# Optimization experiments

Measured on AMD Instinct MI355X. Metric: run time of the kernel, lower is better.

Reference implementation:

```python
import jax, jax.numpy as jnp
import numpy as np

EPS = 1e-7
MAX_TAN_NORM = 10.0  # safe_expmap0 clamp


def logmap0(x):
    # x: [..., D] Lorentz point, x[..., 0] = time component (>= 1)
    x0 = x[..., :1]
    xs = x[..., 1:]
    d = jnp.arccosh(jnp.clip(x0, 1.0 + EPS, None))          # geodesic distance to origin
    ns = jnp.clip(jnp.linalg.norm(xs, axis=-1, keepdims=True), EPS, None)
    return jnp.concatenate([jnp.zeros_like(x0), d * xs / ns], axis=-1)


def safe_expmap0(u):
    # u: tangent at origin; time component is projected out (proju at origin)
    us = u[..., 1:]
    n = jnp.clip(jnp.linalg.norm(us, axis=-1, keepdims=True), EPS, None)
    nc = jnp.minimum(n, MAX_TAN_NORM)                        # clamp norm for stability
    usc = us * (nc / n)
    return jnp.concatenate([jnp.cosh(nc), jnp.sinh(nc) * usc / nc], axis=-1)


def projx(x):
    # re-project onto the hyperboloid: x0 = sqrt(1 + ||xs||^2)
    xs = x[..., 1:]
    x0 = jnp.sqrt(1.0 + jnp.sum(xs * xs, axis=-1, keepdims=True))
    return jnp.concatenate([x0, xs], axis=-1)


def lorentz_linear(x_hyp, W, b):
    t = logmap0(x_hyp)
    y = t @ W.T + b
    return projx(safe_expmap0(y))


def setup_inputs() -> dict:
    key = jax.random.key(0)
    ks = jax.random.split(key, 8)
    N, D_IN, D_HID, D_OUT = 8192, 1024, 4096, 1024
    s = 0.02
    x_sp = jax.random.normal(ks[0], (N, D_IN), dtype=jnp.float32)
    x_hyp = projx(x_sp)  # valid Lorentz point (time comp overwritten)
    W1 = jax.random.normal(ks[1], (D_HID, D_IN), dtype=jnp.float32) * s
    b1 = jnp.zeros((D_HID,), dtype=jnp.float32)
    W2 = jax.random.normal(ks[2], (D_HID, D_HID), dtype=jnp.float32) * s
    b2 = jnp.zeros((D_HID,), dtype=jnp.float32)
    W3 = jax.random.normal(ks[3], (D_OUT, D_HID), dtype=jnp.float32) * s
    b3 = jnp.zeros((D_OUT,), dtype=jnp.float32)
    return {"x_hyp": x_hyp, "W1": W1, "b1": b1, "W2": W2, "b2": b2, "W3": W3, "b3": b3}


def reference(x_hyp, W1, b1, W2, b2, W3, b3):
    # layers[:-1] with inter-layer logmap0 -> (dropout=identity in eval) -> expmap0 -> projx
    h = lorentz_linear(x_hyp, W1, b1)
    h = projx(safe_expmap0(logmap0(h)))
    h = lorentz_linear(h, W2, b2)
    h = projx(safe_expmap0(logmap0(h)))
    return lorentz_linear(h, W3, b3)
```

## Files before the change

### kernel.cpp

```cpp
#include <hip/hip_runtime.h>
#include <stdint.h>

#define EPSF 1e-7f
#define MAXTAN 10.0f

typedef __bf16 bf16x8 __attribute__((ext_vector_type(8)));
typedef float floatx4 __attribute__((ext_vector_type(4)));
typedef __attribute__((address_space(3))) void lds_void_t;
typedef __attribute__((address_space(1))) void gbl_void_t;

__device__ __forceinline__ unsigned short f2bf(float x) {
  union { float f; uint32_t u; } v; v.f = x;
  uint32_t u = v.u;
  u += 0x7fffu + ((u >> 16) & 1u);
  return (unsigned short)(u >> 16);
}
__device__ __forceinline__ float bf2f(unsigned short h) {
  union { uint32_t u; float f; } v; v.u = ((uint32_t)h) << 16;
  return v.f;
}

__global__ void k_sniff(const unsigned short* __restrict__ x, int* __restrict__ mode) {
  if (threadIdx.x == 0 && blockIdx.x == 0) {
    int sane = 0;
    for (int i = 0; i < 128; ++i) {
      unsigned short h = x[i];
      int e = (h >> 7) & 0xFF;
      if ((h & 0x7FFF) == 0 || (e >= 96 && e <= 140)) ++sane;
    }
    *mode = (sane >= 120) ? 1 : 0;
  }
}

__global__ void k_zero(float* __restrict__ p, int n) {
  int i = blockIdx.x * 256 + threadIdx.x;
  if (i < n) p[i] = 0.f;
}

__global__ void k_cvtw(const void* __restrict__ in, unsigned short* __restrict__ out,
                       const int* __restrict__ mode, int n8) {
  int i = blockIdx.x * 256 + threadIdx.x;
  if (i >= n8) return;
  if (*mode) {
    ((uint4*)out)[i] = ((const uint4*)in)[i];
  } else {
    float4 a = ((const float4*)in)[2 * i];
    float4 b = ((const float4*)in)[2 * i + 1];
    ushort4 oa, ob;
    oa.x = f2bf(a.x); oa.y = f2bf(a.y); oa.z = f2bf(a.z); oa.w = f2bf(a.w);
    ob.x = f2bf(b.x); ob.y = f2bf(b.y); ob.z = f2bf(b.z); ob.w = f2bf(b.w);
    ((ushort4*)out)[2 * i] = oa;
    ((ushort4*)out)[2 * i + 1] = ob;
  }
}

__global__ void k_col0(const unsigned short* __restrict__ W, int K,
                       float* __restrict__ out, int n) {
  int i = blockIdx.x * 256 + threadIdx.x;
  if (i < n) out[i] = bf2f(W[(size_t)i * K]);
}

__global__ void k_logmap0(const void* __restrict__ xv, unsigned short* __restrict__ t,
                          const int* __restrict__ mode) {
  const int row = blockIdx.x;
  const int tid = threadIdx.x;
  float4 v; float x0;
  if (*mode) {
    const unsigned short* xr = (const unsigned short*)xv + (size_t)row * 1024;
    ushort4 u = ((const ushort4*)xr)[tid];
    v.x = bf2f(u.x); v.y = bf2f(u.y); v.z = bf2f(u.z); v.w = bf2f(u.w);
    x0 = bf2f(xr[0]);
  } else {
    const float* xr = (const float*)xv + (size_t)row * 1024;
    v = ((const float4*)xr)[tid];
    x0 = xr[0];
  }
  float s = v.x * v.x + v.y * v.y + v.z * v.z + v.w * v.w;
  if (tid == 0) s -= v.x * v.x;
  for (int off = 32; off; off >>= 1) s += __shfl_down(s, off, 64);
  __shared__ float red[4];
  if ((tid & 63) == 0) red[tid >> 6] = s;
  __syncthreads();
  s = red[0] + red[1] + red[2] + red[3];
  float ns = fmaxf(sqrtf(s), EPSF);
  float d = acoshf(fmaxf(x0, 1.0f + EPSF));
  float sc = d / ns;
  ushort4 o;
  o.x = f2bf(v.x * sc); o.y = f2bf(v.y * sc);
  o.z = f2bf(v.z * sc); o.w = f2bf(v.w * sc);
  if (tid == 0) o.x = 0;
  ((ushort4*)(t + (size_t)row * 1024))[tid] = o;
}

__global__ void k_sc(const float* __restrict__ ss, const unsigned short* __restrict__ y,
                     int stride, float* __restrict__ sc, float* __restrict__ c0f, int nrows) {
  int i = blockIdx.x * 256 + threadIdx.x;
  if (i >= nrows) return;
  float n = fmaxf(sqrtf(fmaxf(ss[i], 0.f)), EPSF);
  sc[i] = fminf(n, MAXTAN) / n;
  c0f[i] = bf2f(y[(size_t)i * stride]);
}

__global__ void k_final(const unsigned short* __restrict__ y, const float* __restrict__ ss,
                        void* __restrict__ outv, const int* __restrict__ mode) {
  const int row = blockIdx.x;
  const int tid = threadIdx.x;
  float n = fmaxf(sqrtf(fmaxf(ss[row], 0.f)), EPSF);
  float nc = fminf(n, MAXTAN);
  float a = sinhf(nc) / n;
  ushort4 u = ((const ushort4*)(y + (size_t)row * 1024))[tid];
  float4 o;
  o.x = bf2f(u.x) * a; o.y = bf2f(u.y) * a;
  o.z = bf2f(u.z) * a; o.w = bf2f(u.w) * a;
  if (tid == 0) o.x = coshf(nc);
  if (*mode) {
    ushort4 o16;
    o16.x = f2bf(o.x); o16.y = f2bf(o.y); o16.z = f2bf(o.z); o16.w = f2bf(o.w);
    ((ushort4*)outv)[(size_t)row * 256 + tid] = o16;
  } else {
    ((float4*)outv)[(size_t)row * 256 + tid] = o;
  }
}

template<int N, int K, bool CORR>
__global__ __launch_bounds__(256) void k_gemm_bt(
    const unsigned short* __restrict__ A,
    const unsigned short* __restrict__ B,
    const float* __restrict__ bias,
    const float* __restrict__ sc,
    const float* __restrict__ c0f,
    const float* __restrict__ wc0,
    unsigned short* __restrict__ Cb,
    float* __restrict__ ss)
{
  __shared__ __align__(16) unsigned short As[128 * 64];
  __shared__ __align__(16) unsigned short Bs[128 * 64];

  const int tid  = threadIdx.x;
  const int wave = tid >> 6;
  const int lane = tid & 63;
  const int quad = lane >> 4;
  const int m16  = lane & 15;

  const int bm = blockIdx.y * 128;
  const int bn = blockIdx.x * 128;

  const int srow = lane >> 3;
  const int gcol = (((lane & 7) ^ srow) << 3);

  const int wm = (wave >> 1) << 6;
  const int wn = (wave & 1) << 6;

  floatx4 acc[4][4];
#pragma unroll
  for (int i = 0; i < 4; ++i)
#pragma unroll
    for (int j = 0; j < 4; ++j)
#pragma unroll
      for (int r = 0; r < 4; ++r) acc[i][j][r] = 0.0f;

  for (int k0 = 0; k0 < K; k0 += 64) {
#pragma unroll
    for (int i = 0; i < 4; ++i) {
      const int rbase = wave * 32 + i * 8;
      const unsigned short* ga = A + (size_t)(bm + rbase + srow) * K + k0 + gcol;
      const unsigned short* gb = B + (size_t)(bn + rbase + srow) * K + k0 + gcol;
      __builtin_amdgcn_global_load_lds((gbl_void_t*)(void*)ga,
                                       (lds_void_t*)(As + rbase * 64), 16, 0, 0);
      __builtin_amdgcn_global_load_lds((gbl_void_t*)(void*)gb,
                                       (lds_void_t*)(Bs + rbase * 64), 16, 0, 0);
    }
    __syncthreads();

#pragma unroll
    for (int j = 0; j < 2; ++j) {
      bf16x8 af[4], bfg[4];
#pragma unroll
      for (int t = 0; t < 4; ++t) {
        const int gsw = (((j * 4 + quad) ^ (m16 & 7)) << 3);
        af[t]  = *(const bf16x8*)(As + (wm + t * 16 + m16) * 64 + gsw);
        bfg[t] = *(const bf16x8*)(Bs + (wn + t * 16 + m16) * 64 + gsw);
      }
#pragma unroll
      for (int mt = 0; mt < 4; ++mt)
#pragma unroll
        for (int nt = 0; nt < 4; ++nt)
          acc[mt][nt] = __builtin_amdgcn_mfma_f32_16x16x32_bf16(af[mt], bfg[nt], acc[mt][nt], 0, 0, 0);
    }
    __syncthreads();
  }

#pragma unroll
  for (int mt = 0; mt < 4; ++mt) {
#pragma unroll
    for (int r = 0; r < 4; ++r) {
      const int gm = bm + wm + mt * 16 + quad * 4 + r;
      float scv = 1.f, c0v = 0.f;
      if (CORR) { scv = sc[gm]; c0v = c0f[gm]; }
      float sq = 0.f;
#pragma unroll
      for (int nt = 0; nt < 4; ++nt) {
        const int gn = bn + wn + nt * 16 + m16;
        float v = acc[mt][nt][r];
        if (CORR) v = scv * (v - c0v * wc0[gn]);
        v += bias[gn];
        Cb[(size_t)gm * N + gn] = f2bf(v);
        sq += (gn == 0) ? 0.f : v * v;
      }
      sq += __shfl_xor(sq, 1, 64);
      sq += __shfl_xor(sq, 2, 64);
      sq += __shfl_xor(sq, 4, 64);
      sq += __shfl_xor(sq, 8, 64);
      if (m16 == 0) atomicAdd(&ss[gm], sq);
    }
  }
}

extern "C" void kernel_launch(void* const* d_in, const int* in_sizes, int n_in,
                              void* d_out, int out_size, void* d_ws, size_t ws_size,
                              hipStream_t stream) {
  const void* x  = d_in[0];
  const void* W1 = d_in[1];
  const float* b1 = (const float*)d_in[2];
  const void* W2 = d_in[3];
  const float* b2 = (const float*)d_in[4];
  const void* W3 = d_in[5];
  const float* b3 = (const float*)d_in[6];

  const int NR = 8192, DIN = 1024, DH = 4096, DOUT = 1024;

  char* ws = (char*)d_ws;
  size_t off = 0;
  int* mode = (int*)(ws + off);               off += 256;
  unsigned short* W1b = (unsigned short*)(ws + off); off += (size_t)DH * DIN * 2;
  unsigned short* W2b = (unsigned short*)(ws + off); off += (size_t)DH * DH * 2;
  unsigned short* W3b = (unsigned short*)(ws + off); off += (size_t)DOUT * DH * 2;
  unsigned short* t1  = (unsigned short*)(ws + off); off += (size_t)NR * DIN * 2;
  unsigned short* y1  = (unsigned short*)(ws + off); off += (size_t)NR * DH * 2;
  unsigned short* y2  = (unsigned short*)(ws + off); off += (size_t)NR * DH * 2;
  unsigned short* y3  = (unsigned short*)(ws + off); off += (size_t)NR * DOUT * 2;
  float* ssb  = (float*)(ws + off); off += (size_t)3 * NR * 4;
  float* sc1  = (float*)(ws + off); off += (size_t)NR * 4;
  float* c01  = (float*)(ws + off); off += (size_t)NR * 4;
  float* sc2  = (float*)(ws + off); off += (size_t)NR * 4;
  float* c02  = (float*)(ws + off); off += (size_t)NR * 4;
  float* w2c0 = (float*)(ws + off); off += (size_t)DH * 4;
  float* w3c0 = (float*)(ws + off); off += (size_t)DOUT * 4;
  float* ss1 = ssb, *ss2 = ssb + NR, *ss3 = ssb + 2 * NR;

  k_sniff<<<1, 64, 0, stream>>>((const unsigned short*)x, mode);
  k_zero<<<(3 * NR + 255) / 256, 256, 0, stream>>>(ssb, 3 * NR);

  k_cvtw<<<(DH * DIN / 8 + 255) / 256, 256, 0, stream>>>(W1, W1b, mode, DH * DIN / 8);
  k_cvtw<<<(DH * DH  / 8 + 255) / 256, 256, 0, stream>>>(W2, W2b, mode, DH * DH / 8);
  k_cvtw<<<(DOUT * DH / 8 + 255) / 256, 256, 0, stream>>>(W3, W3b, mode, DOUT * DH / 8);
  k_col0<<<(DH + 255) / 256, 256, 0, stream>>>(W2b, DH, w2c0, DH);
  k_col0<<<(DOUT + 255) / 256, 256, 0, stream>>>(W3b, DH, w3c0, DOUT);

  k_logmap0<<<NR, 256, 0, stream>>>(x, t1, mode);

  k_gemm_bt<4096, 1024, false><<<dim3(DH / 128, NR / 128), 256, 0, stream>>>(
      t1, W1b, b1, nullptr, nullptr, nullptr, y1, ss1);
  k_sc<<<(NR + 255) / 256, 256, 0, stream>>>(ss1, y1, DH, sc1, c01, NR);

  k_gemm_bt<4096, 4096, true><<<dim3(DH / 128, NR / 128), 256, 0, stream>>>(
      y1, W2b, b2, sc1, c01, w2c0, y2, ss2);
  k_sc<<<(NR + 255) / 256, 256, 0, stream>>>(ss2, y2, DH, sc2, c02, NR);

  k_gemm_bt<1024, 4096, true><<<dim3(DOUT / 128, NR / 128), 256, 0, stream>>>(
      y2, W3b, b3, sc2, c02, w3c0, y3, ss3);

  k_final<<<NR, 256, 0, stream>>>(y3, ss3, d_out, mode);
}
```

Baseline: 704.0 us.

## Halve GEMM K-tile, replace atomics with partial sums, fold logmap0 into GEMM

Several changes at once. The GEMM K step drops from 64 to 32 with a new LDS swizzle, which halves shared memory per block and may raise occupancy but doubles the number of barrier iterations. Per-row squared-norm atomics become deterministic per-block partial-sum writes that k_sc reduces. The first layer's logmap0 scaling now goes through the same scale-and-correct epilogue as the other layers, so the kernel only converts x to bf16. Weight column-0 extraction is fused into the weight conversion, and biases are converted to float in their own kernel.

```diff
diff --git a/kernel.cpp b/kernel.cpp
--- a/kernel.cpp
+++ b/kernel.cpp
@@ -32,17 +32,46 @@
   }
 }
 
-__global__ void k_zero(float* __restrict__ p, int n) {
-  int i = blockIdx.x * 256 + threadIdx.x;
-  if (i < n) p[i] = 0.f;
-}
-
+__global__ void k_prep(const void* __restrict__ xv, unsigned short* __restrict__ xb,
+                       float* __restrict__ sc0, float* __restrict__ x0c,
+                       const int* __restrict__ mode) {
+  const int row = blockIdx.x;
+  const int tid = threadIdx.x;
+  float4 v;
+  if (*mode) {
+    ushort4 u = ((const ushort4*)((const unsigned short*)xv + (size_t)row * 1024))[tid];
+    v.x = bf2f(u.x); v.y = bf2f(u.y); v.z = bf2f(u.z); v.w = bf2f(u.w);
+  } else {
+    v = ((const float4*)((const float*)xv + (size_t)row * 1024))[tid];
+  }
+  ushort4 o;
+  o.x = f2bf(v.x); o.y = f2bf(v.y); o.z = f2bf(v.z); o.w = f2bf(v.w);
+  ((ushort4*)(xb + (size_t)row * 1024))[tid] = o;
+
+  float s = v.x * v.x + v.y * v.y + v.z * v.z + v.w * v.w;
+  if (tid == 0) s -= v.x * v.x;
+  for (int off = 32; off; off >>= 1) s += __shfl_down(s, off, 64);
+  __shared__ float red[4];
+  if ((tid & 63) == 0) red[tid >> 6] = s;
+  __syncthreads();
+  if (tid == 0) {
+    s = red[0] + red[1] + red[2] + red[3];
+    float ns = fmaxf(sqrtf(s), EPSF);
+    float d = acoshf(fmaxf(v.x, 1.0f + EPSF));
+    sc0[row] = d / ns;
+    x0c[row] = bf2f(o.x);
+  }
+}
+
+template<int K8>
 __global__ void k_cvtw(const void* __restrict__ in, unsigned short* __restrict__ out,
-                       const int* __restrict__ mode, int n8) {
+                       const int* __restrict__ mode, int n8, float* __restrict__ c0) {
   int i = blockIdx.x * 256 + threadIdx.x;
   if (i >= n8) return;
   if (*mode) {
-    ((uint4*)out)[i] = ((const uint4*)in)[i];
+    uint4 g = ((const uint4*)in)[i];
+    ((uint4*)out)[i] = g;
+    if (i % K8 == 0) c0[i / K8] = bf2f((unsigned short)(g.x & 0xFFFFu));
   } else {
     float4 a = ((const float4*)in)[2 * i];
     float4 b = ((const float4*)in)[2 * i + 1];
@@ -51,54 +80,34 @@
     ob.x = f2bf(b.x); ob.y = f2bf(b.y); ob.z = f2bf(b.z); ob.w = f2bf(b.w);
     ((ushort4*)out)[2 * i] = oa;
     ((ushort4*)out)[2 * i + 1] = ob;
-  }
-}
-
-__global__ void k_col0(const unsigned short* __restrict__ W, int K,
-                       float* __restrict__ out, int n) {
+    if (i % K8 == 0) c0[i / K8] = bf2f(oa.x);
+  }
+}
+
+__global__ void k_cvtb(const void* __restrict__ b1, const void* __restrict__ b2,
+                       const void* __restrict__ b3, float* __restrict__ o1,
+                       float* __restrict__ o2, float* __restrict__ o3,
+                       const int* __restrict__ mode) {
   int i = blockIdx.x * 256 + threadIdx.x;
-  if (i < n) out[i] = bf2f(W[(size_t)i * K]);
-}
-
-__global__ void k_logmap0(const void* __restrict__ xv, unsigned short* __restrict__ t,
-                          const int* __restrict__ mode) {
-  const int row = blockIdx.x;
-  const int tid = threadIdx.x;
-  float4 v; float x0;
-  if (*mode) {
-    const unsigned short* xr = (const unsigned short*)xv + (size_t)row * 1024;
-    ushort4 u = ((const ushort4*)xr)[tid];
-    v.x = bf2f(u.x); v.y = bf2f(u.y); v.z = bf2f(u.z); v.w = bf2f(u.w);
-    x0 = bf2f(xr[0]);
-  } else {
-    const float* xr = (const float*)xv + (size_t)row * 1024;
-    v = ((const float4*)xr)[tid];
-    x0 = xr[0];
-  }
-  float s = v.x * v.x + v.y * v.y + v.z * v.z + v.w * v.w;
-  if (tid == 0) s -= v.x * v.x;
-  for (int off = 32; off; off >>= 1) s += __shfl_down(s, off, 64);
-  __shared__ float red[4];
-  if ((tid & 63) == 0) red[tid >> 6] = s;
-  __syncthreads();
-  s = red[0] + red[1] + red[2] + red[3];
-  float ns = fmaxf(sqrtf(s), EPSF);
-  float d = acoshf(fmaxf(x0, 1.0f + EPSF));
-  float sc = d / ns;
-  ushort4 o;
-  o.x = f2bf(v.x * sc); o.y = f2bf(v.y * sc);
-  o.z = f2bf(v.z * sc); o.w = f2bf(v.w * sc);
-  if (tid == 0) o.x = 0;
-  ((ushort4*)(t + (size_t)row * 1024))[tid] = o;
-}
-
-__global__ void k_sc(const float* __restrict__ ss, const unsigned short* __restrict__ y,
-                     int stride, float* __restrict__ sc, float* __restrict__ c0f, int nrows) {
+  int m = *mode;
+  if (i < 4096) o1[i] = m ? bf2f(((const unsigned short*)b1)[i]) : ((const float*)b1)[i];
+  if (i < 4096) o2[i] = m ? bf2f(((const unsigned short*)b2)[i]) : ((const float*)b2)[i];
+  if (i < 1024) o3[i] = m ? bf2f(((const unsigned short*)b3)[i]) : ((const float*)b3)[i];
+}
+
+template<int NBLK>
+__global__ void k_sc(const float* __restrict__ part, const unsigned short* __restrict__ y,
+                     int stride, float* __restrict__ sc, float* __restrict__ c0,
+                     float* __restrict__ ssout, int nrows) {
   int i = blockIdx.x * 256 + threadIdx.x;
   if (i >= nrows) return;
-  float n = fmaxf(sqrtf(fmaxf(ss[i], 0.f)), EPSF);
+  float s = 0.f;
+#pragma unroll
+  for (int j = 0; j < NBLK; ++j) s += part[(size_t)i * NBLK + j];
+  float n = fmaxf(sqrtf(fmaxf(s, 0.f)), EPSF);
   sc[i] = fminf(n, MAXTAN) / n;
-  c0f[i] = bf2f(y[(size_t)i * stride]);
+  c0[i] = bf2f(y[(size_t)i * stride]);
+  if (ssout) ssout[i] = s;
 }
 
 __global__ void k_final(const unsigned short* __restrict__ y, const float* __restrict__ ss,
@@ -122,7 +131,7 @@
   }
 }
 
-template<int N, int K, bool CORR>
+template<int N, int K, int NBLK>
 __global__ __launch_bounds__(256) void k_gemm_bt(
     const unsigned short* __restrict__ A,
     const unsigned short* __restrict__ B,
@@ -131,10 +140,10 @@
     const float* __restrict__ c0f,
     const float* __restrict__ wc0,
     unsigned short* __restrict__ Cb,
-    float* __restrict__ ss)
+    float* __restrict__ part)
 {
-  __shared__ __align__(16) unsigned short As[128 * 64];
-  __shared__ __align__(16) unsigned short Bs[128 * 64];
+  __shared__ __align__(16) unsigned short As[128 * 32];
+  __shared__ __align__(16) unsigned short Bs[128 * 32];
 
   const int tid  = threadIdx.x;
   const int wave = tid >> 6;
@@ -145,12 +154,14 @@
   const int bm = blockIdx.y * 128;
   const int bn = blockIdx.x * 128;
 
-  const int srow = lane >> 3;
-  const int gcol = (((lane & 7) ^ srow) << 3);
+  const int srow = lane >> 2;
+  const int scol = (((lane & 3) ^ ((srow >> 1) & 3)) << 3);
 
   const int wm = (wave >> 1) << 6;
   const int wn = (wave & 1) << 6;
 
+  const int rsw = ((quad ^ ((m16 >> 1) & 3)) << 3);
+
   floatx4 acc[4][4];
 #pragma unroll
   for (int i = 0; i < 4; ++i)
@@ -159,34 +170,30 @@
 #pragma unroll
       for (int r = 0; r < 4; ++r) acc[i][j][r] = 0.0f;
 
-  for (int k0 = 0; k0 < K; k0 += 64) {
-#pragma unroll
-    for (int i = 0; i < 4; ++i) {
-      const int rbase = wave * 32 + i * 8;
-      const unsigned short* ga = A + (size_t)(bm + rbase + srow) * K + k0 + gcol;
-      const unsigned short* gb = B + (size_t)(bn + rbase + srow) * K + k0 + gcol;
+  for (int k0 = 0; k0 < K; k0 += 32) {
+#pragma unroll
+    for (int i = 0; i < 2; ++i) {
+      const int c = wave * 2 + i;
+      const unsigned short* ga = A + (size_t)(bm + c * 16 + srow) * K + k0 + scol;
+      const unsigned short* gb = B + (size_t)(bn + c * 16 + srow) * K + k0 + scol;
       __builtin_amdgcn_global_load_lds((gbl_void_t*)(void*)ga,
-                                       (lds_void_t*)(As + rbase * 64), 16, 0, 0);
+                                       (lds_void_t*)(As + c * 512), 16, 0, 0);
       __builtin_amdgcn_global_load_lds((gbl_void_t*)(void*)gb,
-                                       (lds_void_t*)(Bs + rbase * 64), 16, 0, 0);
+                                       (lds_void_t*)(Bs + c * 512), 16, 0, 0);
     }
     __syncthreads();
 
-#pragma unroll
-    for (int j = 0; j < 2; ++j) {
-      bf16x8 af[4], bfg[4];
-#pragma unroll
-      for (int t = 0; t < 4; ++t) {
-        const int gsw = (((j * 4 + quad) ^ (m16 & 7)) << 3);
-        af[t]  = *(const bf16x8*)(As + (wm + t * 16 + m16) * 64 + gsw);
-        bfg[t] = *(const bf16x8*)(Bs + (wn + t * 16 + m16) * 64 + gsw);
-      }
-#pragma unroll
-      for (int mt = 0; mt < 4; ++mt)
-#pragma unroll
-        for (int nt = 0; nt < 4; ++nt)
-          acc[mt][nt] = __builtin_amdgcn_mfma_f32_16x16x32_bf16(af[mt], bfg[nt], acc[mt][nt], 0, 0, 0);
-    }
+    bf16x8 af[4], bfg[4];
+#pragma unroll
+    for (int t = 0; t < 4; ++t) {
+      af[t]  = *(const bf16x8*)(As + (wm + t * 16 + m16) * 32 + rsw);
+      bfg[t] = *(const bf16x8*)(Bs + (wn + t * 16 + m16) * 32 + rsw);
+    }
+#pragma unroll
+    for (int mt = 0; mt < 4; ++mt)
+#pragma unroll
+      for (int nt = 0; nt < 4; ++nt)
+        acc[mt][nt] = __builtin_amdgcn_mfma_f32_16x16x32_bf16(af[mt], bfg[nt], acc[mt][nt], 0, 0, 0);
     __syncthreads();
   }
 
@@ -195,15 +202,13 @@
 #pragma unroll
     for (int r = 0; r < 4; ++r) {
       const int gm = bm + wm + mt * 16 + quad * 4 + r;
-      float scv = 1.f, c0v = 0.f;
-      if (CORR) { scv = sc[gm]; c0v = c0f[gm]; }
+      const float scv = sc[gm];
+      const float c0v = c0f[gm];
       float sq = 0.f;
 #pragma unroll
       for (int nt = 0; nt < 4; ++nt) {
         const int gn = bn + wn + nt * 16 + m16;
-        float v = acc[mt][nt][r];
-        if (CORR) v = scv * (v - c0v * wc0[gn]);
-        v += bias[gn];
+        float v = scv * (acc[mt][nt][r] - c0v * wc0[gn]) + bias[gn];
         Cb[(size_t)gm * N + gn] = f2bf(v);
         sq += (gn == 0) ? 0.f : v * v;
       }
@@ -211,7 +216,7 @@
       sq += __shfl_xor(sq, 2, 64);
       sq += __shfl_xor(sq, 4, 64);
       sq += __shfl_xor(sq, 8, 64);
-      if (m16 == 0) atomicAdd(&ss[gm], sq);
+      if (m16 == 0) part[(size_t)gm * NBLK + 2 * blockIdx.x + (wave & 1)] = sq;
     }
   }
 }
@@ -221,54 +226,61 @@
                               hipStream_t stream) {
   const void* x  = d_in[0];
   const void* W1 = d_in[1];
-  const float* b1 = (const float*)d_in[2];
+  const void* b1 = d_in[2];
   const void* W2 = d_in[3];
-  const float* b2 = (const float*)d_in[4];
+  const void* b2 = d_in[4];
   const void* W3 = d_in[5];
-  const float* b3 = (const float*)d_in[6];
+  const void* b3 = d_in[6];
 
   const int NR = 8192, DIN = 1024, DH = 4096, DOUT = 1024;
 
   char* ws = (char*)d_ws;
   size_t off = 0;
-  int* mode = (int*)(ws + off);               off += 256;
-  unsigned short* W1b = (unsigned short*)(ws + off); off += (size_t)DH * DIN * 2;
-  unsigned short* W2b = (unsigned short*)(ws + off); off += (size_t)DH * DH * 2;
-  unsigned short* W3b = (unsigned short*)(ws + off); off += (size_t)DOUT * DH * 2;
-  unsigned short* t1  = (unsigned short*)(ws + off); off += (size_t)NR * DIN * 2;
-  unsigned short* y1  = (unsigned short*)(ws + off); off += (size_t)NR * DH * 2;
-  unsigned short* y2  = (unsigned short*)(ws + off); off += (size_t)NR * DH * 2;
-  unsigned short* y3  = (unsigned short*)(ws + off); off += (size_t)NR * DOUT * 2;
-  float* ssb  = (float*)(ws + off); off += (size_t)3 * NR * 4;
-  float* sc1  = (float*)(ws + off); off += (size_t)NR * 4;
-  float* c01  = (float*)(ws + off); off += (size_t)NR * 4;
-  float* sc2  = (float*)(ws + off); off += (size_t)NR * 4;
-  float* c02  = (float*)(ws + off); off += (size_t)NR * 4;
-  float* w2c0 = (float*)(ws + off); off += (size_t)DH * 4;
-  float* w3c0 = (float*)(ws + off); off += (size_t)DOUT * 4;
-  float* ss1 = ssb, *ss2 = ssb + NR, *ss3 = ssb + 2 * NR;
+  int* mode = (int*)(ws + off);                        off += 256;
+  unsigned short* W1b = (unsigned short*)(ws + off);   off += (size_t)DH * DIN * 2;
+  unsigned short* W2b = (unsigned short*)(ws + off);   off += (size_t)DH * DH * 2;
+  unsigned short* W3b = (unsigned short*)(ws + off);   off += (size_t)DOUT * DH * 2;
+  unsigned short* xb  = (unsigned short*)(ws + off);   off += (size_t)NR * DIN * 2;
+  unsigned short* y1  = (unsigned short*)(ws + off);   off += (size_t)NR * DH * 2;
+  unsigned short* y2  = (unsigned short*)(ws + off);   off += (size_t)NR * DH * 2;
+  unsigned short* y3  = (unsigned short*)(ws + off);   off += (size_t)NR * DOUT * 2;
+  float* part1 = (float*)(ws + off);                   off += (size_t)NR * 64 * 4;
+  float* part2 = (float*)(ws + off);                   off += (size_t)NR * 64 * 4;
+  float* part3 = (float*)(ws + off);                   off += (size_t)NR * 16 * 4;
+  float* sc0  = (float*)(ws + off);                    off += (size_t)NR * 4;
+  float* x0c  = (float*)(ws + off);                    off += (size_t)NR * 4;
+  float* sc1  = (float*)(ws + off);                    off += (size_t)NR * 4;
+  float* c01  = (float*)(ws + off);                    off += (size_t)NR * 4;
+  float* sc2  = (float*)(ws + off);                    off += (size_t)NR * 4;
+  float* c02  = (float*)(ws + off);                    off += (size_t)NR * 4;
+  float* ss3  = (float*)(ws + off);                    off += (size_t)NR * 4;
+  float* w1c0 = (float*)(ws + off);                    off += (size_t)DH * 4;
+  float* w2c0 = (float*)(ws + off);                    off += (size_t)DH * 4;
+  float* w3c0 = (float*)(ws + off);                    off += (size_t)DOUT * 4;
+  float* b1f  = (float*)(ws + off);                    off += (size_t)DH * 4;
+  float* b2f  = (float*)(ws + off);                    off += (size_t)DH * 4;
+  float* b3f  = (float*)(ws + off);                    off += (size_t)DOUT * 4;
 
   k_sniff<<<1, 64, 0, stream>>>((const unsigned short*)x, mode);
-  k_zero<<<(3 * NR + 255) / 256, 256, 0, stream>>>(ssb, 3 * NR);
-
-  k_cvtw<<<(DH * DIN / 8 + 255) / 256, 256, 0, stream>>>(W1, W1b, mode, DH * DIN / 8);
-  k_cvtw<<<(DH * DH  / 8 + 255) / 256, 256, 0, stream>>>(W2, W2b, mode, DH * DH / 8);
-  k_cvtw<<<(DOUT * DH / 8 + 255) / 256, 256, 0, stream>>>(W3, W3b, mode, DOUT * DH / 8);
-  k_col0<<<(DH + 255) / 256, 256, 0, stream>>>(W2b, DH, w2c0, DH);
-  k_col0<<<(DOUT + 255) / 256, 256, 0, stream>>>(W3b, DH, w3c0, DOUT);
-
-  k_logmap0<<<NR, 256, 0, stream>>>(x, t1, mode);
-
-  k_gemm_bt<4096, 1024, false><<<dim3(DH / 128, NR / 128), 256, 0, stream>>>(
-      t1, W1b, b1, nullptr, nullptr, nullptr, y1, ss1);
-  k_sc<<<(NR + 255) / 256, 256, 0, stream>>>(ss1, y1, DH, sc1, c01, NR);
-
-  k_gemm_bt<4096, 4096, true><<<dim3(DH / 128, NR / 128), 256, 0, stream>>>(
-      y1, W2b, b2, sc1, c01, w2c0, y2, ss2);
-  k_sc<<<(NR + 255) / 256, 256, 0, stream>>>(ss2, y2, DH, sc2, c02, NR);
-
-  k_gemm_bt<1024, 4096, true><<<dim3(DOUT / 128, NR / 128), 256, 0, stream>>>(
-      y2, W3b, b3, sc2, c02, w3c0, y3, ss3);
+
+  k_cvtb<<<16, 256, 0, stream>>>(b1, b2, b3, b1f, b2f, b3f, mode);
+  k_cvtw<128><<<(DH * DIN / 8 + 255) / 256, 256, 0, stream>>>(W1, W1b, mode, DH * DIN / 8, w1c0);
+  k_cvtw<512><<<(DH * DH  / 8 + 255) / 256, 256, 0, stream>>>(W2, W2b, mode, DH * DH / 8, w2c0);
+  k_cvtw<512><<<(DOUT * DH / 8 + 255) / 256, 256, 0, stream>>>(W3, W3b, mode, DOUT * DH / 8, w3c0);
+
+  k_prep<<<NR, 256, 0, stream>>>(x, xb, sc0, x0c, mode);
+
+  k_gemm_bt<4096, 1024, 64><<<dim3(DH / 128, NR / 128), 256, 0, stream>>>(
+      xb, W1b, b1f, sc0, x0c, w1c0, y1, part1);
+  k_sc<64><<<(NR + 255) / 256, 256, 0, stream>>>(part1, y1, DH, sc1, c01, nullptr, NR);
+
+  k_gemm_bt<4096, 4096, 64><<<dim3(DH / 128, NR / 128), 256, 0, stream>>>(
+      y1, W2b, b2f, sc1, c01, w2c0, y2, part2);
+  k_sc<64><<<(NR + 255) / 256, 256, 0, stream>>>(part2, y2, DH, sc2, c02, nullptr, NR);
+
+  k_gemm_bt<1024, 4096, 16><<<dim3(DOUT / 128, NR / 128), 256, 0, stream>>>(
+      y2, W3b, b3f, sc2, c02, w3c0, y3, part3);
+  k_sc<16><<<(NR + 255) / 256, 256, 0, stream>>>(part3, y3, DOUT, sc0, x0c, ss3, NR);
 
   k_final<<<NR, 256, 0, stream>>>(y3, ss3, d_out, mode);
 }
```

Measured after the change: 713.9 us. About the same (+1.4%).
